# Performance work log

Hardware: AMD Instinct MI355X
Metric: run time of the kernel (lower is better)

Reference implementation:

```python
import jax, jax.numpy as jnp
import numpy as np

T, B, F, H, P = 256, 512, 256, 512, 12  # seq len, batch, feature_dim, hidden_dim, p_interval


def setup_inputs() -> dict:
    key = jax.random.key(0)
    ks = jax.random.split(key, 9)
    s = 1.0 / np.sqrt(F + H)  # torch Linear default init scale
    def lin(k):
        kw, kb = jax.random.split(k)
        W = jax.random.uniform(kw, (F + H, H), jnp.float32, -s, s)
        b = jax.random.uniform(kb, (H,), jnp.float32, -s, s)
        return W, b
    Wf, bf = lin(ks[0])
    Wi, bi = lin(ks[1])
    Wo, bo = lin(ks[2])
    Wg, bg = lin(ks[3])
    x = jax.random.normal(ks[4], (T, B, F), jnp.float32)
    return {"x": x, "Wf": Wf, "bf": bf, "Wi": Wi, "bi": bi,
            "Wo": Wo, "bo": bo, "Wg": Wg, "bg": bg}


def _slstm(x, Wf, bf, Wi, bi, Wo, bo, Wg, bg):
    Tn, Bn, _ = x.shape
    h0 = jnp.zeros((P, Bn, H), x.dtype)
    # NOTE: original torch code reassigns c to a 2D [B,H] tensor after step 0,
    # so c[t % P] indexes a batch ROW (shape [H]) that broadcasts. At t=0 the
    # slice is all-zeros either way, so carrying a 2D c is exactly faithful.
    c0 = jnp.zeros((Bn, H), x.dtype)

    def step(carry, inp):
        h, c = carry
        x_t, t = inp
        idx = t % P
        xc = jnp.concatenate([x_t, h[idx]], axis=1)  # [B, F+H]
        f = jax.nn.softmax(xc @ Wf + bf, axis=1)
        i = jax.nn.softmax(xc @ Wi + bi, axis=1)
        o = jax.nn.softmax(xc @ Wo + bo, axis=1)
        g = jnp.tanh(xc @ Wg + bg)
        c_new = jnp.tanh(f * c[idx] + i * g)  # c[idx]: row [H], broadcasts over B
        h = h.at[idx].set(o * c_new)
        return (h, c_new), None

    (h, _), _ = jax.lax.scan(step, (h0, c0), (x, jnp.arange(Tn)))
    return h[(Tn - 1) % P]


def reference(x, Wf, bf, Wi, bi, Wo, bo, Wg, bg):
    return _slstm(x, Wf, bf, Wi, bi, Wo, bo, Wg, bg)
```

## Files before the change

kernel.cpp:

```cpp
#include <hip/hip_runtime.h>

typedef unsigned short u16;
typedef unsigned int   u32;

typedef __attribute__((ext_vector_type(8))) short bf16x8;
typedef __attribute__((ext_vector_type(16))) float f32x16;

__device__ __forceinline__ u16 f2bf(float v) {
    u32 u = __float_as_uint(v);
    u32 r = (u + 0x7fffu + ((u >> 16) & 1u)) >> 16;
    return (u16)r;
}
__device__ __forceinline__ float bf2f(u16 h) { return __uint_as_float(((u32)h) << 16); }

__device__ __forceinline__ float ftanh(float x) {
    float e = __expf(2.0f * x);
    return 1.0f - 2.0f * __builtin_amdgcn_rcpf(e + 1.0f);
}

__device__ __forceinline__ void gl2lds16(const void* g, void* l) {
    __builtin_amdgcn_global_load_lds(
        (const __attribute__((address_space(1))) void*)g,
        (__attribute__((address_space(3))) void*)l, 16, 0, 0);
}

__global__ void init_k(u16* __restrict__ hh, u16* __restrict__ hl, float* __restrict__ cb) {
    int i = blockIdx.x * 256 + threadIdx.x;
    hh[i] = 0; hl[i] = 0;
    if (i < 2 * 512) cb[i] = 0.0f;
}

__global__ void pack_wq(const float* __restrict__ Wf, const float* __restrict__ bf_,
                        const float* __restrict__ Wi, const float* __restrict__ bi_,
                        const float* __restrict__ Wo, const float* __restrict__ bo_,
                        const float* __restrict__ Wg, const float* __restrict__ bg_,
                        u16* __restrict__ wq, float* __restrict__ bias4) {
    int idx = blockIdx.x * 256 + threadIdx.x;
    int n = idx / 768, k = idx - n * 768;
    int gate = n >> 9, col = n & 511;
    const float* W = (gate == 0) ? Wf : (gate == 1) ? Wi : (gate == 2) ? Wo : Wg;
    float v = W[k * 512 + col];
    u16 h = f2bf(v);
    u16 l = f2bf(v - bf2f(h));
    size_t base = (size_t)n * 2304;
    if (k < 256) {
        wq[base + k] = h; wq[base + 512 + k] = h; wq[base + 256 + k] = l;
    } else {
        int d = k - 256;
        wq[base + 768 + d] = h; wq[base + 1792 + d] = h; wq[base + 1280 + d] = l;
    }
    if (k == 0) {
        const float* bb = (gate == 0) ? bf_ : (gate == 1) ? bi_ : (gate == 2) ? bo_ : bg_;
        bias4[n] = bb[col];
    }
}

__global__ void split_x(const float* __restrict__ src, u16* __restrict__ oh, u16* __restrict__ ol) {
    int i = blockIdx.x * 256 + threadIdx.x;
    float4 v = ((const float4*)src)[i];
    u16 hx = f2bf(v.x), hy = f2bf(v.y), hz = f2bf(v.z), hw = f2bf(v.w);
    u16 lx = f2bf(v.x - bf2f(hx)), ly = f2bf(v.y - bf2f(hy));
    u16 lz = f2bf(v.z - bf2f(hz)), lw = f2bf(v.w - bf2f(hw));
    uint2 hv; hv.x = (u32)hx | ((u32)hy << 16); hv.y = (u32)hz | ((u32)hw << 16);
    uint2 lv; lv.x = (u32)lx | ((u32)ly << 16); lv.y = (u32)lz | ((u32)lw << 16);
    ((uint2*)oh)[i] = hv;
    ((uint2*)ol)[i] = lv;
}

#define KT 36
__global__ __launch_bounds__(512, 2) void gemm_q(
    const u16* __restrict__ xh, const u16* __restrict__ xl,
    const u16* __restrict__ hh, const u16* __restrict__ hl,
    const u16* __restrict__ wq, const float* __restrict__ bias4,
    float* __restrict__ lg, int Mvalid, int gx) {
    __shared__ __align__(16) u16 smem[69632];

    const int tid = threadIdx.x;
    const int wid = tid >> 6, lane = tid & 63;
    const int l32 = lane & 31, khalf = lane >> 5;
    const int wm = wid >> 2, wn = wid & 3;

    int bm, bn;
    if (gx == 32) { int xcd = blockIdx.x & 7, r = blockIdx.x >> 3; bm = xcd * 4 + (r & 3); bn = r >> 2; }
    else          { bm = blockIdx.x % gx; bn = blockIdx.x / gx; }

    const int lr8 = lane >> 3;
    const int ksw = ((lane & 7) ^ (lr8 & 7)) * 8;

    int arowc[3]; size_t brow[4];
#pragma unroll
    for (int c = 0; c < 3; ++c) {
        int row = bm * 192 + (wid * 3 + c) * 8 + lr8;
        if (row >= Mvalid) row = Mvalid - 1;
        arowc[c] = row;
    }
#pragma unroll
    for (int c = 0; c < 4; ++c)
        brow[c] = (size_t)(bn * 256 + (wid * 4 + c) * 8 + lr8) * 2304;

#define STAGE_A(kt, dstoff) do {                                              \
        int kt_ = (kt); const u16* base_; int str_, ko_;                      \
        if (kt_ < 12) { base_ = (kt_ >= 8) ? xl : xh; str_ = 256; ko_ = (kt_ & 3) * 64; } \
        else { int sub_ = kt_ - 12; base_ = (sub_ >= 16) ? hl : hh; str_ = 512; ko_ = (sub_ & 7) * 64; } \
        _Pragma("unroll")                                                     \
        for (int c_ = 0; c_ < 3; ++c_)                                        \
            gl2lds16(base_ + (size_t)arowc[c_] * str_ + ko_ + ksw,            \
                     smem + (dstoff) + (wid * 3 + c_) * 512 + lane * 8);      \
    } while (0)

#define STAGE_B(kt, dstoff) do {                                              \
        _Pragma("unroll")                                                     \
        for (int c_ = 0; c_ < 4; ++c_)                                        \
            gl2lds16(wq + brow[c_] + (kt) * 64 + ksw,                         \
                     smem + (dstoff) + (wid * 4 + c_) * 512 + lane * 8);      \
    } while (0)

    u32 offA[3][4], offB[2][4];
#pragma unroll
    for (int i = 0; i < 3; ++i) {
        int row = wm * 96 + i * 32 + l32;
        u32 rsw = (u32)(row & 7) << 3;
#pragma unroll
        for (int ks = 0; ks < 4; ++ks)
            offA[i][ks] = (u32)row * 64 + (((u32)(ks * 16 + khalf * 8)) ^ rsw);
    }
#pragma unroll
    for (int j = 0; j < 2; ++j) {
        int row = wn * 64 + j * 32 + l32;
        u32 rsw = (u32)(row & 7) << 3;
#pragma unroll
        for (int ks = 0; ks < 4; ++ks)
            offB[j][ks] = (u32)row * 64 + (((u32)(ks * 16 + khalf * 8)) ^ rsw);
    }

    f32x16 acc[3][2];
#pragma unroll
    for (int i = 0; i < 3; ++i)
#pragma unroll
        for (int j = 0; j < 2; ++j)
#pragma unroll
            for (int r = 0; r < 16; ++r) acc[i][j][r] = 0.f;

#define RD(S, p) do {                                                         \
        S##A0 = *(const bf16x8*)(At + offA[0][p]);                            \
        S##A1 = *(const bf16x8*)(At + offA[1][p]);                            \
        S##A2 = *(const bf16x8*)(At + offA[2][p]);                            \
        S##B0 = *(const bf16x8*)(Bt + offB[0][p]);                            \
        S##B1 = *(const bf16x8*)(Bt + offB[1][p]);                            \
    } while (0)
#define MM(S) do {                                                            \
        __builtin_amdgcn_s_setprio(1);                                        \
        acc[0][0] = __builtin_amdgcn_mfma_f32_32x32x16_bf16(S##A0, S##B0, acc[0][0], 0, 0, 0); \
        acc[0][1] = __builtin_amdgcn_mfma_f32_32x32x16_bf16(S##A0, S##B1, acc[0][1], 0, 0, 0); \
        acc[1][0] = __builtin_amdgcn_mfma_f32_32x32x16_bf16(S##A1, S##B0, acc[1][0], 0, 0, 0); \
        acc[1][1] = __builtin_amdgcn_mfma_f32_32x32x16_bf16(S##A1, S##B1, acc[1][1], 0, 0, 0); \
        acc[2][0] = __builtin_amdgcn_mfma_f32_32x32x16_bf16(S##A2, S##B0, acc[2][0], 0, 0, 0); \
        acc[2][1] = __builtin_amdgcn_mfma_f32_32x32x16_bf16(S##A2, S##B1, acc[2][1], 0, 0, 0); \
        __builtin_amdgcn_s_setprio(0);                                        \
    } while (0)

    STAGE_A(0, 0);
    STAGE_B(0, 36864);
    STAGE_A(1, 12288);
    asm volatile("s_waitcnt vmcnt(3)" ::: "memory");
    asm volatile("s_barrier" ::: "memory");
    __builtin_amdgcn_sched_barrier(0);

#pragma unroll 6
    for (int kt = 0; kt < KT; ++kt) {
        const u16* At = smem + (kt % 3) * 12288;
        const u16* Bt = smem + 36864 + (kt & 1) * 16384;
        const int bdst = 36864 + (((kt + 1) & 1) << 14);
        const int adst = ((kt + 2) % 3) * 12288;

        bf16x8 saA0, saA1, saA2, saB0, saB1;
        bf16x8 sbA0, sbA1, sbA2, sbB0, sbB1;
        bf16x8 scA0, scA1, scA2, scB0, scB1;

        RD(sa, 0);
        if (kt + 1 < KT) STAGE_B(kt + 1, bdst);
        RD(sb, 1);
        if (kt + 2 < KT) STAGE_A(kt + 2, adst);
        MM(sa);
        RD(sc, 2);
        MM(sb);
        RD(sa, 3);
        MM(sc);
        MM(sa);

        if (kt < KT - 2) asm volatile("s_waitcnt vmcnt(3)" ::: "memory");
        else             asm volatile("s_waitcnt vmcnt(0)" ::: "memory");
        asm volatile("s_barrier" ::: "memory");
        __builtin_amdgcn_sched_barrier(0);
    }
#undef STAGE_A
#undef STAGE_B
#undef RD
#undef MM

#pragma unroll
    for (int j = 0; j < 2; ++j) {
        int n = bn * 256 + wn * 64 + j * 32 + l32;
        float bv = bias4[n];
#pragma unroll
        for (int i = 0; i < 3; ++i) {
            int rbase = bm * 192 + wm * 96 + i * 32 + 4 * khalf;
#pragma unroll
            for (int r = 0; r < 16; ++r) {
                int row = rbase + (r & 3) + 8 * (r >> 2);
                if (row < Mvalid)
                    lg[(size_t)row * 2048 + n] = acc[i][j][r] + bv;
            }
        }
    }
}

__device__ __forceinline__ void chain_step(const float* __restrict__ lg, int j, int lane, float r[8]) {
    int rowb = (j + 1) % 12;
    const float* base = lg + (size_t)(j * 512 + rowb) * 2048 + lane * 8;
    float f[8], iv[8], g[8];
#pragma unroll
    for (int u = 0; u < 8; ++u) { f[u] = base[u]; iv[u] = base[512 + u]; g[u] = base[1536 + u]; }
    float mf = -1e30f, mi = -1e30f;
#pragma unroll
    for (int u = 0; u < 8; ++u) { mf = fmaxf(mf, f[u]); mi = fmaxf(mi, iv[u]); }
#pragma unroll
    for (int o = 32; o; o >>= 1) { mf = fmaxf(mf, __shfl_xor(mf, o)); mi = fmaxf(mi, __shfl_xor(mi, o)); }
    float sf = 0.f, si = 0.f;
#pragma unroll
    for (int u = 0; u < 8; ++u) {
        f[u] = __expf(f[u] - mf); sf += f[u];
        iv[u] = __expf(iv[u] - mi); si += iv[u];
    }
#pragma unroll
    for (int o = 32; o; o >>= 1) { sf += __shfl_xor(sf, o); si += __shfl_xor(si, o); }
    float rf = __builtin_amdgcn_rcpf(sf), ri = __builtin_amdgcn_rcpf(si);
#pragma unroll
    for (int u = 0; u < 8; ++u) {
        float gg = ftanh(g[u]);
        r[u] = ftanh(f[u] * rf * r[u] + iv[u] * ri * gg);
    }
}

__global__ __launch_bounds__(256) void gates_k(
    const float* __restrict__ lg, float* __restrict__ cb,
    u16* __restrict__ hh, u16* __restrict__ hl,
    float* __restrict__ out, int t0, int S, int rd, int wr) {
    __shared__ float rsh[512];
    const int widx = threadIdx.x >> 6, lane = threadIdx.x & 63;
    const int s = (S - 1) - (blockIdx.x >> 7);
    const int b = (blockIdx.x & 127) * 4 + widx;
    const int t = t0 + s;

    if (widx == 0) {
        float r[8];
#pragma unroll
        for (int u = 0; u < 8; ++u) r[u] = cb[rd * 512 + lane * 8 + u];
        for (int j = 0; j < s; ++j) chain_step(lg, j, lane, r);
#pragma unroll
        for (int u = 0; u < 8; ++u) rsh[lane * 8 + u] = r[u];
        if ((int)blockIdx.x == 127 && t0 + S < 256) {
            chain_step(lg, S - 1, lane, r);
#pragma unroll
            for (int u = 0; u < 8; ++u) cb[wr * 512 + lane * 8 + u] = r[u];
        }
    }
    __syncthreads();

    const float* row = lg + (size_t)(s * 512 + b) * 2048 + lane * 8;
    float f[8], iv[8], ov[8], g[8];
#pragma unroll
    for (int u = 0; u < 8; ++u) {
        f[u] = row[u]; iv[u] = row[512 + u]; ov[u] = row[1024 + u]; g[u] = row[1536 + u];
    }
    float mf = -1e30f, mi = -1e30f, mo = -1e30f;
#pragma unroll
    for (int u = 0; u < 8; ++u) { mf = fmaxf(mf, f[u]); mi = fmaxf(mi, iv[u]); mo = fmaxf(mo, ov[u]); }
#pragma unroll
    for (int o = 32; o; o >>= 1) {
        mf = fmaxf(mf, __shfl_xor(mf, o));
        mi = fmaxf(mi, __shfl_xor(mi, o));
        mo = fmaxf(mo, __shfl_xor(mo, o));
    }
    float sf = 0.f, si = 0.f, so = 0.f;
#pragma unroll
    for (int u = 0; u < 8; ++u) {
        f[u] = __expf(f[u] - mf); sf += f[u];
        iv[u] = __expf(iv[u] - mi); si += iv[u];
        ov[u] = __expf(ov[u] - mo); so += ov[u];
    }
#pragma unroll
    for (int o = 32; o; o >>= 1) {
        sf += __shfl_xor(sf, o); si += __shfl_xor(si, o); so += __shfl_xor(so, o);
    }
    float rf = __builtin_amdgcn_rcpf(sf), ri = __builtin_amdgcn_rcpf(si), ro = __builtin_amdgcn_rcpf(so);
    float hout[8];
#pragma unroll
    for (int u = 0; u < 8; ++u) {
        float rr = rsh[lane * 8 + u];
        float gg = ftanh(g[u]);
        float cv = ftanh(f[u] * rf * rr + iv[u] * ri * gg);
        hout[u] = ov[u] * ro * cv;
    }
    u32 hhp[4], hlp[4];
#pragma unroll
    for (int u = 0; u < 4; ++u) {
        u16 h0 = f2bf(hout[2 * u]), h1 = f2bf(hout[2 * u + 1]);
        u16 l0 = f2bf(hout[2 * u] - bf2f(h0)), l1 = f2bf(hout[2 * u + 1] - bf2f(h1));
        hhp[u] = (u32)h0 | ((u32)h1 << 16);
        hlp[u] = (u32)l0 | ((u32)l1 << 16);
    }
    size_t hb = ((size_t)(s * 512 + b)) * 512 + lane * 8;
    *(uint4*)&hh[hb] = make_uint4(hhp[0], hhp[1], hhp[2], hhp[3]);
    *(uint4*)&hl[hb] = make_uint4(hlp[0], hlp[1], hlp[2], hlp[3]);
    if (t == 255) {
        float* op = out + (size_t)b * 512 + lane * 8;
#pragma unroll
        for (int u = 0; u < 8; ++u) op[u] = hout[u];
    }
}

extern "C" void kernel_launch(void* const* d_in, const int* in_sizes, int n_in,
                              void* d_out, int out_size, void* d_ws, size_t ws_size,
                              hipStream_t stream) {
    const float* x   = (const float*)d_in[0];
    const float* Wf  = (const float*)d_in[1];
    const float* bf_ = (const float*)d_in[2];
    const float* Wi  = (const float*)d_in[3];
    const float* bi_ = (const float*)d_in[4];
    const float* Wo  = (const float*)d_in[5];
    const float* bo_ = (const float*)d_in[6];
    const float* Wg  = (const float*)d_in[7];
    const float* bg_ = (const float*)d_in[8];
    float* out = (float*)d_out;

    char* p = (char*)d_ws;
    u16* xh  = (u16*)p; p += 134217728;
    u16* xl  = (u16*)p; p += 134217728;
    u16* wq  = (u16*)p; p += 9437184;
    u16* hh  = (u16*)p; p += 6291456;
    u16* hl  = (u16*)p; p += 6291456;
    float* bias4 = (float*)p; p += 8192;
    float* cb    = (float*)p; p += 4096;
    float* lg    = (float*)p; p += 50331648;

    init_k<<<12288, 256, 0, stream>>>(hh, hl, cb);
    pack_wq<<<6144, 256, 0, stream>>>(Wf, bf_, Wi, bi_, Wo, bo_, Wg, bg_, wq, bias4);
    split_x<<<32768, 256, 0, stream>>>(x, xh, xl);

    for (int blk = 0; blk < 22; ++blk) {
        int t0 = blk * 12;
        int S = (256 - t0 >= 12) ? 12 : (256 - t0);
        int M = S * 512;
        int gx = (M + 191) / 192;
        gemm_q<<<gx * 8, 512, 0, stream>>>(
            xh + (size_t)t0 * 512 * 256, xl + (size_t)t0 * 512 * 256,
            hh, hl, wq, bias4, lg, M, gx);
        gates_k<<<S * 128, 256, 0, stream>>>(lg, cb, hh, hl, out, t0, S, blk & 1, (blk + 1) & 1);
    }
}
```

Baseline: 1.991 ms.

## Halve GEMM K-tile and use a 4-stage unified LDS ring with register prefetch

Changes the gemm_q main loop from 64-wide K tiles (36 iterations, triple-buffered A and double-buffered B) to 32-wide K tiles (72 iterations) held in a 4-deep ring where A and B share one stage index. Each iteration issues the loads for stage kt+3 and reads the LDS fragments for the next tile into registers while the current MFMAs run. The swizzle and the global-to-LDS staging layout are redone for the narrower tile. The aim is deeper load latency hiding and smaller LDS use, paid for with twice as many barriers and waitcnts per K.

```diff
diff --git a/kernel.cpp b/kernel.cpp
--- a/kernel.cpp
+++ b/kernel.cpp
@@ -67,13 +67,13 @@
     ((uint2*)ol)[i] = lv;
 }
 
-#define KT 36
+#define KT 72
 __global__ __launch_bounds__(512, 2) void gemm_q(
     const u16* __restrict__ xh, const u16* __restrict__ xl,
     const u16* __restrict__ hh, const u16* __restrict__ hl,
     const u16* __restrict__ wq, const float* __restrict__ bias4,
     float* __restrict__ lg, int Mvalid, int gx) {
-    __shared__ __align__(16) u16 smem[69632];
+    __shared__ __align__(16) u16 smem[57344];
 
     const int tid = threadIdx.x;
     const int wid = tid >> 6, lane = tid & 63;
@@ -84,54 +84,44 @@
     if (gx == 32) { int xcd = blockIdx.x & 7, r = blockIdx.x >> 3; bm = xcd * 4 + (r & 3); bn = r >> 2; }
     else          { bm = blockIdx.x % gx; bn = blockIdx.x / gx; }
 
-    const int lr8 = lane >> 3;
-    const int ksw = ((lane & 7) ^ (lr8 & 7)) * 8;
-
-    int arowc[3]; size_t brow[4];
-#pragma unroll
-    for (int c = 0; c < 3; ++c) {
-        int row = bm * 192 + (wid * 3 + c) * 8 + lr8;
-        if (row >= Mvalid) row = Mvalid - 1;
-        arowc[c] = row;
-    }
-#pragma unroll
-    for (int c = 0; c < 4; ++c)
-        brow[c] = (size_t)(bn * 256 + (wid * 4 + c) * 8 + lr8) * 2304;
-
-#define STAGE_A(kt, dstoff) do {                                              \
-        int kt_ = (kt); const u16* base_; int str_, ko_;                      \
-        if (kt_ < 12) { base_ = (kt_ >= 8) ? xl : xh; str_ = 256; ko_ = (kt_ & 3) * 64; } \
-        else { int sub_ = kt_ - 12; base_ = (sub_ >= 16) ? hl : hh; str_ = 512; ko_ = (sub_ & 7) * 64; } \
-        _Pragma("unroll")                                                     \
-        for (int c_ = 0; c_ < 3; ++c_)                                        \
-            gl2lds16(base_ + (size_t)arowc[c_] * str_ + ko_ + ksw,            \
-                     smem + (dstoff) + (wid * 3 + c_) * 512 + lane * 8);      \
+    const int rl  = lane >> 2;
+    const int bq  = lane & 3;
+    const int rlh = rl >> 3;
+    const int cA0 = wid;
+    const int cA1 = (wid < 4) ? 8 + wid : wid;
+    const int cB0 = 2 * wid, cB1 = 2 * wid + 1;
+
+    int arow0 = bm * 192 + cA0 * 16 + rl; if (arow0 >= Mvalid) arow0 = Mvalid - 1;
+    int arow1 = bm * 192 + cA1 * 16 + rl; if (arow1 >= Mvalid) arow1 = Mvalid - 1;
+    const int ak0 = (bq ^ ((2 * cA0 + rlh) & 3)) * 8;
+    const int ak1 = (bq ^ ((2 * cA1 + rlh) & 3)) * 8;
+    const size_t brow0 = (size_t)(bn * 256 + cB0 * 16 + rl) * 2304;
+    const size_t brow1 = (size_t)(bn * 256 + cB1 * 16 + rl) * 2304;
+    const int bk0 = (bq ^ ((2 * cB0 + rlh) & 3)) * 8;
+    const int bk1 = (bq ^ ((2 * cB1 + rlh) & 3)) * 8;
+    const u32 ldsA0 = (u32)cA0 * 512 + (u32)lane * 8;
+    const u32 ldsA1 = (u32)cA1 * 512 + (u32)lane * 8;
+    const u32 ldsB0 = (u32)cB0 * 512 + (u32)lane * 8;
+    const u32 ldsB1 = (u32)cB1 * 512 + (u32)lane * 8;
+
+#define STAGE(kt_, ao_, bo_) do {                                             \
+        int k_ = (kt_); const u16* ab_; int astr_, ako_;                      \
+        if (k_ < 24) { ab_ = (k_ >= 16) ? xl : xh; astr_ = 256; ako_ = (k_ & 7) * 32; } \
+        else { int sub_ = k_ - 24; ab_ = (sub_ >= 32) ? hl : hh; astr_ = 512; ako_ = (sub_ & 15) * 32; } \
+        gl2lds16(ab_ + (size_t)arow0 * astr_ + ako_ + ak0, smem + (ao_) + ldsA0); \
+        gl2lds16(ab_ + (size_t)arow1 * astr_ + ako_ + ak1, smem + (ao_) + ldsA1); \
+        gl2lds16(wq + brow0 + (size_t)k_ * 32 + bk0, smem + (bo_) + ldsB0);   \
+        gl2lds16(wq + brow1 + (size_t)k_ * 32 + bk1, smem + (bo_) + ldsB1);   \
     } while (0)
 
-#define STAGE_B(kt, dstoff) do {                                              \
-        _Pragma("unroll")                                                     \
-        for (int c_ = 0; c_ < 4; ++c_)                                        \
-            gl2lds16(wq + brow[c_] + (kt) * 64 + ksw,                         \
-                     smem + (dstoff) + (wid * 4 + c_) * 512 + lane * 8);      \
-    } while (0)
-
-    u32 offA[3][4], offB[2][4];
-#pragma unroll
-    for (int i = 0; i < 3; ++i) {
-        int row = wm * 96 + i * 32 + l32;
-        u32 rsw = (u32)(row & 7) << 3;
-#pragma unroll
-        for (int ks = 0; ks < 4; ++ks)
-            offA[i][ks] = (u32)row * 64 + (((u32)(ks * 16 + khalf * 8)) ^ rsw);
-    }
-#pragma unroll
-    for (int j = 0; j < 2; ++j) {
-        int row = wn * 64 + j * 32 + l32;
-        u32 rsw = (u32)(row & 7) << 3;
-#pragma unroll
-        for (int ks = 0; ks < 4; ++ks)
-            offB[j][ks] = (u32)row * 64 + (((u32)(ks * 16 + khalf * 8)) ^ rsw);
-    }
+    const u32 swzr = (u32)(l32 >> 3);
+    u32 rowA[3], rowB[2], xk[2];
+#pragma unroll
+    for (int i = 0; i < 3; ++i) rowA[i] = (u32)(wm * 96 + i * 32 + l32) * 32;
+#pragma unroll
+    for (int j = 0; j < 2; ++j) rowB[j] = (u32)(wn * 64 + j * 32 + l32) * 32;
+#pragma unroll
+    for (int ks = 0; ks < 2; ++ks) xk[ks] = (((u32)(ks * 2 + khalf)) ^ swzr) << 3;
 
     f32x16 acc[3][2];
 #pragma unroll
@@ -141,12 +131,15 @@
 #pragma unroll
             for (int r = 0; r < 16; ++r) acc[i][j][r] = 0.f;
 
-#define RD(S, p) do {                                                         \
-        S##A0 = *(const bf16x8*)(At + offA[0][p]);                            \
-        S##A1 = *(const bf16x8*)(At + offA[1][p]);                            \
-        S##A2 = *(const bf16x8*)(At + offA[2][p]);                            \
-        S##B0 = *(const bf16x8*)(Bt + offB[0][p]);                            \
-        S##B1 = *(const bf16x8*)(Bt + offB[1][p]);                            \
+    bf16x8 s0A0, s0A1, s0A2, s0B0, s0B1;
+    bf16x8 s1A0, s1A1, s1A2, s1B0, s1B1;
+
+#define RD(S, ao_, bo_, ks_) do {                                             \
+        S##A0 = *(const bf16x8*)(smem + (ao_) + rowA[0] + xk[ks_]);           \
+        S##A1 = *(const bf16x8*)(smem + (ao_) + rowA[1] + xk[ks_]);           \
+        S##A2 = *(const bf16x8*)(smem + (ao_) + rowA[2] + xk[ks_]);           \
+        S##B0 = *(const bf16x8*)(smem + (bo_) + rowB[0] + xk[ks_]);           \
+        S##B1 = *(const bf16x8*)(smem + (bo_) + rowB[1] + xk[ks_]);           \
     } while (0)
 #define MM(S) do {                                                            \
         __builtin_amdgcn_s_setprio(1);                                        \
@@ -159,44 +152,44 @@
         __builtin_amdgcn_s_setprio(0);                                        \
     } while (0)
 
-    STAGE_A(0, 0);
-    STAGE_B(0, 36864);
-    STAGE_A(1, 12288);
-    asm volatile("s_waitcnt vmcnt(3)" ::: "memory");
+#define AB(r) ((r) * 6144)
+#define BB(r) (24576 + (r) * 8192)
+
+    STAGE(0, AB(0), BB(0));
+    STAGE(1, AB(1), BB(1));
+    STAGE(2, AB(2), BB(2));
+    asm volatile("s_waitcnt vmcnt(4)" ::: "memory");
     asm volatile("s_barrier" ::: "memory");
     __builtin_amdgcn_sched_barrier(0);
-
-#pragma unroll 6
-    for (int kt = 0; kt < KT; ++kt) {
-        const u16* At = smem + (kt % 3) * 12288;
-        const u16* Bt = smem + 36864 + (kt & 1) * 16384;
-        const int bdst = 36864 + (((kt + 1) & 1) << 14);
-        const int adst = ((kt + 2) % 3) * 12288;
-
-        bf16x8 saA0, saA1, saA2, saB0, saB1;
-        bf16x8 sbA0, sbA1, sbA2, sbB0, sbB1;
-        bf16x8 scA0, scA1, scA2, scB0, scB1;
-
-        RD(sa, 0);
-        if (kt + 1 < KT) STAGE_B(kt + 1, bdst);
-        RD(sb, 1);
-        if (kt + 2 < KT) STAGE_A(kt + 2, adst);
-        MM(sa);
-        RD(sc, 2);
-        MM(sb);
-        RD(sa, 3);
-        MM(sc);
-        MM(sa);
-
-        if (kt < KT - 2) asm volatile("s_waitcnt vmcnt(3)" ::: "memory");
-        else             asm volatile("s_waitcnt vmcnt(0)" ::: "memory");
-        asm volatile("s_barrier" ::: "memory");
-        __builtin_amdgcn_sched_barrier(0);
-    }
-#undef STAGE_A
-#undef STAGE_B
+    RD(s0, AB(0), BB(0), 0);
+    RD(s1, AB(0), BB(0), 1);
+
+#define BODY(kt_, RC, RN, RS) do {                                            \
+        if ((kt_) + 3 < KT) STAGE((kt_) + 3, AB(RS), BB(RS));                 \
+        MM(s0);                                                               \
+        RD(s0, AB(RN), BB(RN), 0);                                            \
+        MM(s1);                                                               \
+        RD(s1, AB(RN), BB(RN), 1);                                            \
+        if ((kt_) + 3 < KT) asm volatile("s_waitcnt vmcnt(4)" ::: "memory");  \
+        else                asm volatile("s_waitcnt vmcnt(0)" ::: "memory");  \
+        asm volatile("s_barrier" ::: "memory");                               \
+        __builtin_amdgcn_sched_barrier(0);                                    \
+    } while (0)
+
+#pragma unroll 1
+    for (int q = 0; q < 18; ++q) {
+        int ktb = q * 4;
+        BODY(ktb + 0, 0, 1, 3);
+        BODY(ktb + 1, 1, 2, 0);
+        BODY(ktb + 2, 2, 3, 1);
+        BODY(ktb + 3, 3, 0, 2);
+    }
+#undef BODY
+#undef STAGE
 #undef RD
 #undef MM
+#undef AB
+#undef BB
 
 #pragma unroll
     for (int j = 0; j < 2; ++j) {
```

Result: slower. 2.142 ms (+7.6%).
